# Kernel optimization log

Measured on AMD Instinct MI355X. Metric: run time of the kernel, lower is better.

The kernel has to match this reference:

```python
import jax, jax.numpy as jnp
import numpy as np

B, S, IN, OUT = 4, 2048, 4096, 16384

def setup_inputs() -> dict:
    key = jax.random.key(0)
    k1, k2, k3, k4 = jax.random.split(key, 4)
    x = jax.random.normal(k1, (B, S, IN), dtype=jnp.float32)
    quantized_weight = jax.random.randint(k2, (OUT, IN), 0, 16, dtype=jnp.int32)
    scale = jax.random.uniform(k3, (OUT,), dtype=jnp.float32)
    zero_point = jax.random.randint(k4, (OUT,), 0, 16, dtype=jnp.int32)
    return {"x": x, "quantized_weight": quantized_weight, "scale": scale, "zero_point": zero_point}

def reference(x, quantized_weight, scale, zero_point):
    # Per-output-channel dequantization: W = (q - zp) * scale, shape [OUT, IN]
    weight = (quantized_weight.astype(jnp.float32) - zero_point.astype(jnp.float32)[:, None]) * scale[:, None]
    # F.linear(x, W) = x @ W.T -> [B, S, OUT]
    return jnp.einsum('bsi,oi->bso', x, weight)
```

## Files before the change

### kernel.cpp

```cpp
#include <hip/hip_runtime.h>
#include <stdint.h>

#define MDIM 8192
#define NDIM 16384
#define KDIM 4096
#define NT   64

typedef __attribute__((ext_vector_type(4)))  int i32x4;
typedef __attribute__((ext_vector_type(16))) int i32x16;

__device__ __forceinline__ void gload_lds16(const void* g, void* l) {
    __builtin_amdgcn_global_load_lds(
        (const __attribute__((address_space(1))) void*)g,
        (__attribute__((address_space(3))) void*)l,
        16, 0, 0);
}

__device__ __forceinline__ i32x16 MFMA32(i32x4 a, i32x4 b, i32x16 c) {
    return __builtin_amdgcn_mfma_i32_32x32x32_i8(a, b, c, 0, 0, 0);
}


__global__ __launch_bounds__(256)
void quant_x_kernel(const float* __restrict__ x, int8_t* __restrict__ xq,
                    float* __restrict__ sx) {
    const int row = (int)blockIdx.x;
    const float* xr = x + (long)row * KDIM;
    const int t = threadIdx.x;
    float v[16];
#pragma unroll
    for (int i = 0; i < 4; ++i)
        *(float4*)&v[i * 4] = ((const float4*)xr)[t + 256 * i];
    float m = 0.f;
#pragma unroll
    for (int i = 0; i < 16; ++i) m = fmaxf(m, fabsf(v[i]));
#pragma unroll
    for (int off = 32; off >= 1; off >>= 1) m = fmaxf(m, __shfl_xor(m, off));
    __shared__ float red[4];
    if ((t & 63) == 0) red[t >> 6] = m;
    __syncthreads();
    m = fmaxf(fmaxf(red[0], red[1]), fmaxf(red[2], red[3]));
    m = fmaxf(m, 1e-20f);
    const float inv = 127.0f / m;
    if (t == 0) sx[row] = m * (1.0f / 127.0f);
    int* qo = (int*)(xq + (long)row * KDIM);
#pragma unroll
    for (int i = 0; i < 4; ++i) {
        union { int8_t c[4]; int w; } o;
#pragma unroll
        for (int j = 0; j < 4; ++j)
            o.c[j] = (int8_t)__float2int_rn(v[i * 4 + j] * inv);
        qo[t + 256 * i] = o.w;
    }
}

__global__ __launch_bounds__(256)
void quant_w_kernel(const int* __restrict__ q, const int* __restrict__ zp,
                    int8_t* __restrict__ wq) {
    const long i = (long)blockIdx.x * 256 + threadIdx.x;
    const long e = i * 16;
    const int o = (int)(e >> 12);
    const int z = zp[o];
    union { int8_t c[16]; int4 v; } r;
#pragma unroll
    for (int b = 0; b < 4; ++b) {
        int4 a = ((const int4*)(q + e))[b];
        r.c[b * 4 + 0] = (int8_t)(a.x - z);
        r.c[b * 4 + 1] = (int8_t)(a.y - z);
        r.c[b * 4 + 2] = (int8_t)(a.z - z);
        r.c[b * 4 + 3] = (int8_t)(a.w - z);
    }
    *(int4*)(wq + e) = r.v;
}


__global__ __launch_bounds__(512, 2)
void gemm_i8_kernel(const int8_t* __restrict__ A, const int8_t* __restrict__ Wt,
                    const float* __restrict__ scale, const float* __restrict__ sx,
                    float* __restrict__ C) {
    __shared__ int8_t lds[3 * 32768];

    const int wg = (int)blockIdx.x;
    const int rr = wg >> 8;
    const int ii = wg & 255;
    const int bm = ii & 31;
    const int bn = rr * 8 + (ii >> 5);

    const int tid  = threadIdx.x;
    const int lane = tid & 63;
    const int wid  = tid >> 6;
    const int wm   = wid >> 2;
    const int wn   = wid & 3;
    const int l31  = lane & 31;
    const int lh   = lane >> 5;

    const int xnib = (l31 >> 1) & 3;

    const int s0 = tid, s1 = 512 + tid;
    const int soff0 = (s0 >> 2) * KDIM + ((((s0 & 3) ^ ((s0 >> 3) & 3))) << 4);
    const int soff1 = (s1 >> 2) * KDIM + ((((s1 & 3) ^ ((s1 >> 3) & 3))) << 4);
    const int d0 = s0 * 16, d1 = s1 * 16;

    const int8_t* Ab = A  + (long)bm * 256 * KDIM;
    const int8_t* Wb = Wt + (long)bn * 256 * KDIM;

#define STAGE(bb, P, base, tt)                                                      \
    do {                                                                            \
        gload_lds16((base) + soff0 + (tt) * 64, &lds[(bb) + (P) * 16384 + d0]);     \
        gload_lds16((base) + soff1 + (tt) * 64, &lds[(bb) + (P) * 16384 + d1]);     \
    } while (0)

#define RDA2(DST, BB, MTB)                                                          \
    _Pragma("unroll")                                                               \
    for (int m_ = 0; m_ < 2; ++m_)                                                  \
        _Pragma("unroll")                                                           \
        for (int k_ = 0; k_ < 2; ++k_)                                              \
            DST[m_ * 2 + k_] = *(const i32x4*)&lds[(BB) +                           \
                (wm * 128 + ((MTB) + m_) * 32 + l31) * 64 +                         \
                (((k_ * 2 + lh) ^ xnib) << 4)];

#define RDB(DST, BB)                                                                \
    _Pragma("unroll")                                                               \
    for (int n_ = 0; n_ < 2; ++n_)                                                  \
        _Pragma("unroll")                                                           \
        for (int k_ = 0; k_ < 2; ++k_)                                              \
            DST[n_ * 2 + k_] = *(const i32x4*)&lds[(BB) + 16384 +                   \
                (wn * 64 + n_ * 32 + l31) * 64 +                                    \
                (((k_ * 2 + lh) ^ xnib) << 4)];

#define MFH(MB, AS, BS)                                                             \
    do {                                                                            \
        __builtin_amdgcn_sched_barrier(0);                                          \
        __builtin_amdgcn_s_setprio(1);                                              \
        _Pragma("unroll")                                                           \
        for (int m_ = 0; m_ < 2; ++m_)                                              \
            _Pragma("unroll")                                                       \
            for (int n_ = 0; n_ < 2; ++n_)                                          \
                _Pragma("unroll")                                                   \
                for (int k_ = 0; k_ < 2; ++k_)                                      \
                    acc[(MB) + m_][n_] = MFMA32(AS[m_ * 2 + k_], BS[n_ * 2 + k_],   \
                                                acc[(MB) + m_][n_]);                \
        __builtin_amdgcn_s_setprio(0);                                              \
        __builtin_amdgcn_sched_barrier(0);                                          \
    } while (0)

    i32x16 acc[4][2];
#pragma unroll
    for (int i = 0; i < 4; ++i)
#pragma unroll
        for (int j = 0; j < 2; ++j)
#pragma unroll
            for (int r = 0; r < 16; ++r) acc[i][j][r] = 0;

    i32x4 aS0[4], aHi[4], bSA[4], bSB[4];
    int b0 = 0, b1 = 32768, b2 = 65536;

    STAGE(b0, 0, Ab, 0); STAGE(b0, 1, Wb, 0);
    STAGE(b1, 0, Ab, 1); STAGE(b1, 1, Wb, 1);
    asm volatile("s_waitcnt vmcnt(4)" ::: "memory");
    __builtin_amdgcn_s_barrier();
    RDA2(aS0, b0, 0);
    RDB(bSA, b0);

#define KSTEP(T, BCUR, BNXT)                                                        \
    do {                                                                            \
        const bool pf_ = (T) < NT - 2;                                              \
                   \
        RDA2(aHi, b0, 2);                                                           \
        if (pf_) { STAGE(b2, 0, Ab, (T) + 2); }                                     \
        MFH(0, aS0, BCUR);                                                          \
               \
        asm volatile("s_waitcnt lgkmcnt(0)" ::: "memory");                          \
        if (pf_) asm volatile("s_waitcnt vmcnt(2)" ::: "memory");                   \
        else     asm volatile("s_waitcnt vmcnt(0)" ::: "memory");                   \
        __builtin_amdgcn_s_barrier();                                               \
        RDA2(aS0, b1, 0);                                                           \
        RDB(BNXT, b1);                                                              \
        if (pf_) { STAGE(b2, 1, Wb, (T) + 2); }                                     \
        MFH(2, aHi, BCUR);                                                          \
        const int tb_ = b0; b0 = b1; b1 = b2; b2 = tb_;                             \
    } while (0)

    for (int t = 0; t < NT; t += 2) {
        KSTEP(t,     bSA, bSB);
        KSTEP(t + 1, bSB, bSA);
    }
#undef KSTEP
#undef STAGE
#undef RDA2
#undef RDB
#undef MFH

    const long rowA0 = (long)bm * 256 + wm * 128;
    const int  colB0 = bn * 256 + wn * 64;
    float scj[2];
#pragma unroll
    for (int n = 0; n < 2; ++n) scj[n] = scale[colB0 + n * 32 + l31];
#pragma unroll
    for (int mt = 0; mt < 4; ++mt) {
#pragma unroll
        for (int g = 0; g < 4; ++g) {
            const long rb = rowA0 + mt * 32 + g * 8 + lh * 4;
            const float4 s4 = *(const float4*)(sx + rb);
#pragma unroll
            for (int n = 0; n < 2; ++n) {
                float* cp = C + rb * NDIM + colB0 + n * 32 + l31;
                cp[0 * (long)NDIM] = (float)acc[mt][n][g * 4 + 0] * scj[n] * s4.x;
                cp[1 * (long)NDIM] = (float)acc[mt][n][g * 4 + 1] * scj[n] * s4.y;
                cp[2 * (long)NDIM] = (float)acc[mt][n][g * 4 + 2] * scj[n] * s4.z;
                cp[3 * (long)NDIM] = (float)acc[mt][n][g * 4 + 3] * scj[n] * s4.w;
            }
        }
    }
}


__global__ __launch_bounds__(256)
void fallback_kernel(const float* __restrict__ x, const int* __restrict__ q,
                     const float* __restrict__ scale, const int* __restrict__ zp,
                     float* __restrict__ out) {
    __shared__ float sA[64][17];
    __shared__ float sB[64][17];
    const int bn = (int)blockIdx.x % (NDIM / 64);
    const int bm = (int)blockIdx.x / (NDIM / 64);
    const int t  = threadIdx.x;
    const int tx = t & 15, ty = t >> 4;
    const long rowA = (long)bm * 64, rowB = (long)bn * 64;
    float acc[4][4] = {};
    for (int k0 = 0; k0 < KDIM; k0 += 16) {
#pragma unroll
        for (int i = 0; i < 4; ++i) {
            const int e = t + i * 256;
            const int r = e >> 4, c = e & 15;
            sA[r][c] = x[(rowA + r) * KDIM + k0 + c];
            const int o = (int)rowB + r;
            sB[r][c] = (float)(q[(long)o * KDIM + k0 + c] - zp[o]) * scale[o];
        }
        __syncthreads();
#pragma unroll
        for (int kk = 0; kk < 16; ++kk) {
            float a[4], b[4];
#pragma unroll
            for (int i = 0; i < 4; ++i) a[i] = sA[ty * 4 + i][kk];
#pragma unroll
            for (int j = 0; j < 4; ++j) b[j] = sB[tx * 4 + j][kk];
#pragma unroll
            for (int i = 0; i < 4; ++i)
#pragma unroll
                for (int j = 0; j < 4; ++j) acc[i][j] += a[i] * b[j];
        }
        __syncthreads();
    }
#pragma unroll
    for (int i = 0; i < 4; ++i) {
        const long r = rowA + ty * 4 + i;
#pragma unroll
        for (int j = 0; j < 4; ++j)
            out[r * NDIM + rowB + tx * 4 + j] = acc[i][j];
    }
}


extern "C" void kernel_launch(void* const* d_in, const int* in_sizes, int n_in,
                              void* d_out, int out_size, void* d_ws, size_t ws_size,
                              hipStream_t stream) {
    const float* x     = (const float*)d_in[0];
    const int*   qw    = (const int*)d_in[1];
    const float* scale = (const float*)d_in[2];
    const int*   zp    = (const int*)d_in[3];
    float*       out   = (float*)d_out;

    const size_t needA  = (size_t)MDIM * KDIM;
    const size_t needW  = (size_t)NDIM * KDIM;
    const size_t needSx = (size_t)MDIM * sizeof(float);

    if (ws_size >= needA + needW + needSx) {
        int8_t* xq = (int8_t*)d_ws;
        int8_t* wq = xq + needA;
        float*  sx = (float*)((char*)d_ws + needA + needW);
        quant_x_kernel<<<MDIM, 256, 0, stream>>>(x, xq, sx);
        quant_w_kernel<<<(NDIM * (KDIM / 16)) / 256, 256, 0, stream>>>(qw, zp, wq);
        gemm_i8_kernel<<<(MDIM / 256) * (NDIM / 256), 512, 0, stream>>>(xq, wq, scale, sx, out);
    } else {
        fallback_kernel<<<(MDIM / 64) * (NDIM / 64), 256, 0, stream>>>(x, qw, scale, zp, out);
    }
}
```

Measured before the change: 717.8 us.

## Pre-tile quantized operands into GEMM-native blocked layout for contiguous LDS staging

The quantization kernels now write int8 X and W in a blocked layout (per 256-row panel, per 64-wide K tile, in 16-byte K chunks), so each GEMM stage loads one contiguous 16KB block. This removes the XOR swizzle and the strided global addressing in the LDS staging and fragment reads. X quantization is split into a row-max pass and a separate transposing quantize pass, which reads x twice. The new write pattern has each thread reading 64 contiguous bytes per row, which may coalesce worse, and LDS fragment reads without the swizzle may hit more bank conflicts.

```diff
diff --git a/kernel.cpp b/kernel.cpp
--- a/kernel.cpp
+++ b/kernel.cpp
@@ -5,6 +5,7 @@
 #define NDIM 16384
 #define KDIM 4096
 #define NT   64
+#define PSTR 1048576
 
 typedef __attribute__((ext_vector_type(4)))  int i32x4;
 typedef __attribute__((ext_vector_type(16))) int i32x16;
@@ -22,18 +23,17 @@
 
 
 __global__ __launch_bounds__(256)
-void quant_x_kernel(const float* __restrict__ x, int8_t* __restrict__ xq,
-                    float* __restrict__ sx) {
+void rowmax_kernel(const float* __restrict__ x, float* __restrict__ sx,
+                   float* __restrict__ invx) {
     const int row = (int)blockIdx.x;
-    const float* xr = x + (long)row * KDIM;
+    const float4* xr = (const float4*)(x + (long)row * KDIM);
     const int t = threadIdx.x;
-    float v[16];
-#pragma unroll
-    for (int i = 0; i < 4; ++i)
-        *(float4*)&v[i * 4] = ((const float4*)xr)[t + 256 * i];
     float m = 0.f;
 #pragma unroll
-    for (int i = 0; i < 16; ++i) m = fmaxf(m, fabsf(v[i]));
+    for (int i = 0; i < 4; ++i) {
+        float4 v = xr[t + 256 * i];
+        m = fmaxf(m, fmaxf(fmaxf(fabsf(v.x), fabsf(v.y)), fmaxf(fabsf(v.z), fabsf(v.w))));
+    }
 #pragma unroll
     for (int off = 32; off >= 1; off >>= 1) m = fmaxf(m, __shfl_xor(m, off));
     __shared__ float red[4];
@@ -41,36 +41,49 @@
     __syncthreads();
     m = fmaxf(fmaxf(red[0], red[1]), fmaxf(red[2], red[3]));
     m = fmaxf(m, 1e-20f);
-    const float inv = 127.0f / m;
-    if (t == 0) sx[row] = m * (1.0f / 127.0f);
-    int* qo = (int*)(xq + (long)row * KDIM);
-#pragma unroll
-    for (int i = 0; i < 4; ++i) {
-        union { int8_t c[4]; int w; } o;
-#pragma unroll
-        for (int j = 0; j < 4; ++j)
-            o.c[j] = (int8_t)__float2int_rn(v[i * 4 + j] * inv);
-        qo[t + 256 * i] = o.w;
-    }
-}
-
-__global__ __launch_bounds__(256)
-void quant_w_kernel(const int* __restrict__ q, const int* __restrict__ zp,
-                    int8_t* __restrict__ wq) {
-    const long i = (long)blockIdx.x * 256 + threadIdx.x;
-    const long e = i * 16;
-    const int o = (int)(e >> 12);
+    if (t == 0) { sx[row] = m * (1.0f / 127.0f); invx[row] = 127.0f / m; }
+}
+
+__global__ __launch_bounds__(256)
+void quantx_t_kernel(const float* __restrict__ x, const float* __restrict__ invx,
+                     int8_t* __restrict__ xq) {
+    const int b  = (int)blockIdx.x;
+    const int p  = b >> 8, tt = (b >> 2) & 63, c = b & 3;
+    const int pr = threadIdx.x;
+    const long row = (long)p * 256 + pr;
+    const float inv = invx[row];
+    const float4* src = (const float4*)(x + row * KDIM + tt * 64 + c * 16);
+    union { int8_t ch[16]; int4 v; } r;
+#pragma unroll
+    for (int j = 0; j < 4; ++j) {
+        float4 v = src[j];
+        r.ch[j * 4 + 0] = (int8_t)__float2int_rn(v.x * inv);
+        r.ch[j * 4 + 1] = (int8_t)__float2int_rn(v.y * inv);
+        r.ch[j * 4 + 2] = (int8_t)__float2int_rn(v.z * inv);
+        r.ch[j * 4 + 3] = (int8_t)__float2int_rn(v.w * inv);
+    }
+    *(int4*)(xq + (long)p * PSTR + tt * 16384 + c * 4096 + pr * 16) = r.v;
+}
+
+__global__ __launch_bounds__(256)
+void quantw_t_kernel(const int* __restrict__ q, const int* __restrict__ zp,
+                     int8_t* __restrict__ wq) {
+    const int b  = (int)blockIdx.x;
+    const int p  = b >> 8, tt = (b >> 2) & 63, c = b & 3;
+    const int pr = threadIdx.x;
+    const long o = (long)p * 256 + pr;
     const int z = zp[o];
-    union { int8_t c[16]; int4 v; } r;
-#pragma unroll
-    for (int b = 0; b < 4; ++b) {
-        int4 a = ((const int4*)(q + e))[b];
-        r.c[b * 4 + 0] = (int8_t)(a.x - z);
-        r.c[b * 4 + 1] = (int8_t)(a.y - z);
-        r.c[b * 4 + 2] = (int8_t)(a.z - z);
-        r.c[b * 4 + 3] = (int8_t)(a.w - z);
-    }
-    *(int4*)(wq + e) = r.v;
+    const int4* src = (const int4*)(q + o * KDIM + tt * 64 + c * 16);
+    union { int8_t ch[16]; int4 v; } r;
+#pragma unroll
+    for (int j = 0; j < 4; ++j) {
+        int4 a = src[j];
+        r.ch[j * 4 + 0] = (int8_t)(a.x - z);
+        r.ch[j * 4 + 1] = (int8_t)(a.y - z);
+        r.ch[j * 4 + 2] = (int8_t)(a.z - z);
+        r.ch[j * 4 + 3] = (int8_t)(a.w - z);
+    }
+    *(int4*)(wq + (long)p * PSTR + tt * 16384 + c * 4096 + pr * 16) = r.v;
 }
 
 
@@ -94,20 +107,15 @@
     const int l31  = lane & 31;
     const int lh   = lane >> 5;
 
-    const int xnib = (l31 >> 1) & 3;
-
-    const int s0 = tid, s1 = 512 + tid;
-    const int soff0 = (s0 >> 2) * KDIM + ((((s0 & 3) ^ ((s0 >> 3) & 3))) << 4);
-    const int soff1 = (s1 >> 2) * KDIM + ((((s1 & 3) ^ ((s1 >> 3) & 3))) << 4);
-    const int d0 = s0 * 16, d1 = s1 * 16;
-
-    const int8_t* Ab = A  + (long)bm * 256 * KDIM;
-    const int8_t* Wb = Wt + (long)bn * 256 * KDIM;
+    const int dl = tid * 16;
+
+    const int8_t* Ab = A  + (long)bm * PSTR;
+    const int8_t* Wb = Wt + (long)bn * PSTR;
 
 #define STAGE(bb, P, base, tt)                                                      \
     do {                                                                            \
-        gload_lds16((base) + soff0 + (tt) * 64, &lds[(bb) + (P) * 16384 + d0]);     \
-        gload_lds16((base) + soff1 + (tt) * 64, &lds[(bb) + (P) * 16384 + d1]);     \
+        gload_lds16((base) + (tt) * 16384 + dl,        &lds[(bb) + (P) * 16384 + dl]);        \
+        gload_lds16((base) + (tt) * 16384 + 8192 + dl, &lds[(bb) + (P) * 16384 + 8192 + dl]); \
     } while (0)
 
 #define RDA2(DST, BB, MTB)                                                          \
@@ -115,9 +123,8 @@
     for (int m_ = 0; m_ < 2; ++m_)                                                  \
         _Pragma("unroll")                                                           \
         for (int k_ = 0; k_ < 2; ++k_)                                              \
-            DST[m_ * 2 + k_] = *(const i32x4*)&lds[(BB) +                           \
-                (wm * 128 + ((MTB) + m_) * 32 + l31) * 64 +                         \
-                (((k_ * 2 + lh) ^ xnib) << 4)];
+            DST[m_ * 2 + k_] = *(const i32x4*)&lds[(BB) + ((k_ * 2 + lh) << 12) +   \
+                ((wm * 128 + ((MTB) + m_) * 32 + l31) << 4)];
 
 #define RDB(DST, BB)                                                                \
     _Pragma("unroll")                                                               \
@@ -125,8 +132,7 @@
         _Pragma("unroll")                                                           \
         for (int k_ = 0; k_ < 2; ++k_)                                              \
             DST[n_ * 2 + k_] = *(const i32x4*)&lds[(BB) + 16384 +                   \
-                (wn * 64 + n_ * 32 + l31) * 64 +                                    \
-                (((k_ * 2 + lh) ^ xnib) << 4)];
+                ((k_ * 2 + lh) << 12) + ((wn * 64 + n_ * 32 + l31) << 4)];
 
 #define MFH(MB, AS, BS)                                                             \
     do {                                                                            \
@@ -273,13 +279,16 @@
     const size_t needA  = (size_t)MDIM * KDIM;
     const size_t needW  = (size_t)NDIM * KDIM;
     const size_t needSx = (size_t)MDIM * sizeof(float);
-
-    if (ws_size >= needA + needW + needSx) {
+    const size_t needIx = (size_t)MDIM * sizeof(float);
+
+    if (ws_size >= needA + needW + needSx + needIx) {
         int8_t* xq = (int8_t*)d_ws;
         int8_t* wq = xq + needA;
         float*  sx = (float*)((char*)d_ws + needA + needW);
-        quant_x_kernel<<<MDIM, 256, 0, stream>>>(x, xq, sx);
-        quant_w_kernel<<<(NDIM * (KDIM / 16)) / 256, 256, 0, stream>>>(qw, zp, wq);
+        float*  ix = sx + MDIM;
+        rowmax_kernel<<<MDIM, 256, 0, stream>>>(x, sx, ix);
+        quantx_t_kernel<<<(MDIM / 256) * 64 * 4, 256, 0, stream>>>(x, ix, xq);
+        quantw_t_kernel<<<(NDIM / 256) * 64 * 4, 256, 0, stream>>>(qw, zp, wq);
         gemm_i8_kernel<<<(MDIM / 256) * (NDIM / 256), 512, 0, stream>>>(xq, wq, scale, sx, out);
     } else {
         fallback_kernel<<<(MDIM / 64) * (NDIM / 64), 256, 0, stream>>>(x, qw, scale, zp, out);
```

Result: slower. 775.5 us (+8.0%).
